# Performance work log

Hardware: AMD Instinct MI355X
Metric: run time of the kernel (lower is better)

Reference implementation:

```python
import jax, jax.numpy as jnp
from jax import lax
import numpy as np


def _lstm_scan(x, mask, w_ih, w_hh, b_ih, b_hh):
    # x: [S,B,E], mask: [S,B] bool. torch LSTM gate order: i,f,g,o.
    S, B, _ = x.shape
    H = w_hh.shape[1]
    def step(carry, inp):
        h, c = carry
        xt, mt = inp
        g = xt @ w_ih.T + h @ w_hh.T + b_ih + b_hh
        i, f, gg, o = jnp.split(g, 4, axis=-1)
        c_new = jax.nn.sigmoid(f) * c + jax.nn.sigmoid(i) * jnp.tanh(gg)
        h_new = jax.nn.sigmoid(o) * jnp.tanh(c_new)
        m = mt[:, None]
        return (jnp.where(m, h_new, h), jnp.where(m, c_new, c)), jnp.where(m, h_new, 0.0)
    init = (jnp.zeros((B, H), x.dtype), jnp.zeros((B, H), x.dtype))
    _, hs = lax.scan(step, init, (x, mask))
    return hs  # [S,B,H], zero at padded positions (matches pad_packed_sequence)


def _crf_nll(emissions, tags, mask, start, end, trans):
    # torchcrf CRF (batch_first) negative log-likelihood, reduction='sum'.
    em = jnp.transpose(emissions, (1, 0, 2))  # [S,B,T]
    tg = tags.T                                # [S,B]
    mk = mask.T                                # [S,B] bool
    B = em.shape[1]
    bidx = jnp.arange(B)
    # numerator: gold path score
    score0 = start[tg[0]] + em[0, bidx, tg[0]]
    def num_step(carry, inp):
        score, prev = carry
        e_t, t_t, m_t = inp
        s = score + (trans[prev, t_t] + e_t[bidx, t_t]) * m_t.astype(score.dtype)
        prev2 = jnp.where(m_t, t_t, prev)
        return (s, prev2), None
    (score, last), _ = lax.scan(num_step, (score0, tg[0]), (em[1:], tg[1:], mk[1:]))
    num = score + end[last]
    # denominator: forward algorithm (log partition)
    def den_step(alpha, inp):
        e_t, m_t = inp
        nxt = jax.nn.logsumexp(alpha[:, :, None] + trans[None] + e_t[:, None, :], axis=1)
        return jnp.where(m_t[:, None], nxt, alpha), None
    alpha, _ = lax.scan(den_step, start[None] + em[0], (em[1:], mk[1:]))
    den = jax.nn.logsumexp(alpha + end[None], axis=1)
    return jnp.sum(den - num)  # model returns -llh (sum over batch)


def setup_inputs() -> dict:
    key = jax.random.key(0)
    ks = jax.random.split(key, 20)
    B, S, V, E, H, T = 128, 512, 50000, 256, 512, 32
    sc = 0.05
    sents = jax.random.randint(ks[0], (B, S), 0, V)
    lengths = jax.random.randint(ks[1], (B,), 1, S + 1).at[0].set(S)
    tags = jax.random.randint(ks[2], (B, S), 0, T)
    mask = jnp.arange(S)[None, :] < lengths[:, None]
    return {
        "sents_tensor": sents,
        "lengths": lengths,
        "tags": tags,
        "mask": mask,
        "emb_table": jax.random.normal(ks[3], (V, E), jnp.float32) * sc,
        "w_ih_f": jax.random.normal(ks[4], (4 * H, E), jnp.float32) * sc,
        "w_hh_f": jax.random.normal(ks[5], (4 * H, H), jnp.float32) * sc,
        "b_ih_f": jax.random.normal(ks[6], (4 * H,), jnp.float32) * sc,
        "b_hh_f": jax.random.normal(ks[7], (4 * H,), jnp.float32) * sc,
        "w_ih_b": jax.random.normal(ks[8], (4 * H, E), jnp.float32) * sc,
        "w_hh_b": jax.random.normal(ks[9], (4 * H, H), jnp.float32) * sc,
        "b_ih_b": jax.random.normal(ks[10], (4 * H,), jnp.float32) * sc,
        "b_hh_b": jax.random.normal(ks[11], (4 * H,), jnp.float32) * sc,
        "lin_w": jax.random.normal(ks[12], (T, 2 * H), jnp.float32) * sc,
        "lin_b": jax.random.normal(ks[13], (T,), jnp.float32) * sc,
        "start_trans": jax.random.uniform(ks[14], (T,), jnp.float32, -0.1, 0.1),
        "end_trans": jax.random.uniform(ks[15], (T,), jnp.float32, -0.1, 0.1),
        "transitions": jax.random.uniform(ks[16], (T, T), jnp.float32, -0.1, 0.1),
    }


def reference(sents_tensor, lengths, tags, mask, emb_table,
              w_ih_f, w_hh_f, b_ih_f, b_hh_f,
              w_ih_b, w_hh_b, b_ih_b, b_hh_b,
              lin_w, lin_b, start_trans, end_trans, transitions):
    B, S = sents_tensor.shape
    emb = emb_table[sents_tensor]              # [B,S,E]
    xs = jnp.transpose(emb, (1, 0, 2))         # [S,B,E]
    mk = mask.T                                # [S,B]
    hs_f = _lstm_scan(xs, mk, w_ih_f, w_hh_f, b_ih_f, b_hh_f)
    # backward direction of packed BiLSTM: reverse each sequence within its length
    t = jnp.arange(S)[None, :]
    rev = jnp.where(t < lengths[:, None], lengths[:, None] - 1 - t, t)  # [B,S]
    x_rev = jnp.take_along_axis(emb, rev[:, :, None], axis=1)
    hs_b_rev = _lstm_scan(jnp.transpose(x_rev, (1, 0, 2)), mk, w_ih_b, w_hh_b, b_ih_b, b_hh_b)
    hs_b = jnp.take_along_axis(jnp.transpose(hs_b_rev, (1, 0, 2)), rev[:, :, None], axis=1)
    h = jnp.concatenate([jnp.transpose(hs_f, (1, 0, 2)), hs_b], axis=-1)  # [B,S,2H]
    # dropout in eval mode = identity
    logits = h @ lin_w.T + lin_b               # [B,S,T]
    return _crf_nll(logits, tags, mask, start_trans, end_trans, transitions)
```

## Files before the change

kernel.cpp:

```cpp
#include <hip/hip_runtime.h>
#include <hip/hip_bf16.h>
#include <cstdint>
#include <cstddef>

typedef __bf16 bf16;
typedef __bf16 bf16x8 __attribute__((ext_vector_type(8)));
typedef float f32x4 __attribute__((ext_vector_type(4)));

#define B_ 128
#define S_ 512
#define E_ 256
#define H_ 512

#define EMB_OFF   0UL
#define EMB_SZ    (128UL*512*256*2)
#define HSF_OFF   (EMB_OFF + EMB_SZ)
#define HS_SZ     (512UL*128*512*2)
#define HSB_OFF   (HSF_OFF + HS_SZ)
#define LOG_OFF   (HSB_OFF + HS_SZ)
#define LOG_SZ    (512UL*128*32*4)
#define HPING_OFF (LOG_OFF + LOG_SZ)
#define HPING_SZ  (16UL*2*16*512*2)
#define WLIN_OFF  (HPING_OFF + HPING_SZ)
#define WLIN_SZ   (32UL*1024*2)
#define BAR_OFF   ((WLIN_OFF + WLIN_SZ + 255UL) & ~255UL)
#define BAR_SZ    (16UL*16*32*4)

#define LD_AG(p)    __hip_atomic_load((p),  __ATOMIC_RELAXED, __HIP_MEMORY_SCOPE_AGENT)
#define ST_AG(p,v)  __hip_atomic_store((p), (v), __ATOMIC_RELAXED, __HIP_MEMORY_SCOPE_AGENT)

__device__ __forceinline__ float fsig(float x)  { return 1.0f / (1.0f + __expf(-x)); }
__device__ __forceinline__ float ftanhf(float x){ return 1.0f - 2.0f / (__expf(2.0f * x) + 1.0f); }

__global__ void embed_gather(const int* __restrict__ sents,
                             const float* __restrict__ table,
                             bf16* __restrict__ emb) {
    int t = threadIdx.x;
    int row = blockIdx.x * 8 + (t >> 5);
    int e0 = (t & 31) * 8;
    int idx = sents[row];
    const float4* src = (const float4*)(table + (size_t)idx * 256 + e0);
    float4 f0 = src[0], f1 = src[1];
    bf16x8 v;
    v[0]=(bf16)f0.x; v[1]=(bf16)f0.y; v[2]=(bf16)f0.z; v[3]=(bf16)f0.w;
    v[4]=(bf16)f1.x; v[5]=(bf16)f1.y; v[6]=(bf16)f1.z; v[7]=(bf16)f1.w;
    *(bf16x8*)(emb + (size_t)row * 256 + e0) = v;
}

__global__ void conv_linw(const float* __restrict__ w, bf16* __restrict__ o) {
    int i = blockIdx.x * 256 + threadIdx.x;
    o[i] = (bf16)w[i];
}

__global__ __launch_bounds__(256, 1) void lstm_persistent(
    const bf16* __restrict__ emb, bf16* __restrict__ hping,
    bf16* __restrict__ hs_f, bf16* __restrict__ hs_b,
    const float* __restrict__ w_ih_f, const float* __restrict__ w_hh_f,
    const float* __restrict__ b_ih_f, const float* __restrict__ b_hh_f,
    const float* __restrict__ w_ih_b, const float* __restrict__ w_hh_b,
    const float* __restrict__ b_ih_b, const float* __restrict__ b_hh_b,
    const int* __restrict__ lengths, int* __restrict__ bar)
{
    const int tid = threadIdx.x;
    const int l   = tid & 63;
    const int wv  = tid >> 6;
    const int bid = blockIdx.x;
    const int slot = bid >> 3;
    const int g  = (bid & 7) + ((slot >> 4) << 3);
    const int k  = slot & 15;
    const int d  = g >> 3;
    const int bg = g & 7;
    const int U0 = k * 32;

    const float* Wih = d ? w_ih_b : w_ih_f;
    const float* Whh = d ? w_hh_b : w_hh_f;
    const float* Bih = d ? b_ih_b : b_ih_f;
    const float* Bhh = d ? b_hh_b : b_hh_f;

    __shared__ uint4 smemA[1536];
    __shared__ float gatesS[16 * 132];
    __shared__ float c_sh[512];
    __shared__ float h_sh[512];
    __shared__ int   sh_tmax;

    bf16x8 wf[24][2];
    {
        const int lane15 = l & 15, q = l >> 4;
        #pragma unroll
        for (int kk = 0; kk < 24; ++kk) {
            #pragma unroll
            for (int T = 0; T < 2; ++T) {
                int c   = T * 16 + lane15;
                int row = (c >> 3) * 512 + U0 + 8 * wv + (c & 7);
                int k0  = kk * 32 + q * 8;
                const float* src = (k0 < 256) ? (Wih + (size_t)row * 256 + k0)
                                              : (Whh + (size_t)row * 512 + (k0 - 256));
                float4 f0 = *(const float4*)src;
                float4 f1 = *(const float4*)(src + 4);
                bf16x8 v;
                v[0]=(bf16)f0.x; v[1]=(bf16)f0.y; v[2]=(bf16)f0.z; v[3]=(bf16)f0.w;
                v[4]=(bf16)f1.x; v[5]=(bf16)f1.y; v[6]=(bf16)f1.z; v[7]=(bf16)f1.w;
                wf[kk][T] = v;
            }
        }
    }

    const int uu = tid & 31;
    const int ub = tid >> 5;
    float bI, bF, bG, bO;
    {
        int r0 = U0 + uu;
        bI = Bih[r0]        + Bhh[r0];
        bF = Bih[512 + r0]  + Bhh[512 + r0];
        bG = Bih[1024 + r0] + Bhh[1024 + r0];
        bO = Bih[1536 + r0] + Bhh[1536 + r0];
    }
    int lenU0 = lengths[bg * 16 + ub * 2];
    int lenU1 = lengths[bg * 16 + ub * 2 + 1];

    const int sr  = tid & 15;
    const int sc0 = tid >> 4;
    const int lenR = lengths[bg * 16 + sr];
    const bf16* embB = emb + ((size_t)(bg * 16 + sr)) * 512 * 256;

    for (int i = tid; i < 512; i += 256) { c_sh[i] = 0.0f; h_sh[i] = 0.0f; }
    bf16* hp = hping + (size_t)g * (2 * 16 * 512);
    {
        int r = tid >> 4, cc = tid & 15;
        unsigned int* p = (unsigned int*)(hp + r * 512 + U0 + cc * 2);
        ST_AG(p, 0u);
    }
    if (tid == 0) {
        int mx = 0;
        for (int b2 = 0; b2 < 16; ++b2) mx = max(mx, lengths[bg * 16 + b2]);
        sh_tmax = mx;
    }
    __builtin_amdgcn_s_waitcnt(0x0f70);
    __syncthreads();
    const int tmax = sh_tmax;

    int* slots  = bar + g * 16 * 32;
    int* myslot = slots + k * 32;
    int* pollp  = slots + (tid & 15) * 32;
    if (tid == 0) ST_AG(myslot, 1);

    const int sig = 4 * (l & 15) + (l >> 4);

    for (int t = 0; t < tmax; ++t) {
        bf16* hcur = hp + (t & 1) * (16 * 512);
        bf16* hnxt = hp + ((t + 1) & 1) * (16 * 512);

        int pos = (d == 0) ? t : ((t < lenR) ? (lenR - 1 - t) : t);
        const bf16* xsrc = embB + (size_t)pos * 256;
        #pragma unroll
        for (int i = 0; i < 2; ++i) {
            int c = sc0 + 16 * i;
            uint4 v = *(const uint4*)(xsrc + c * 8);
            smemA[((c >> 2) << 6) + 4 * sr + (c & 3)] = v;
        }

        if (tid < 16) {
            while (LD_AG(pollp) < t + 1) {}
        }
        __syncthreads();

        #pragma unroll
        for (int i = 2; i < 6; ++i) {
            int c = sc0 + 16 * i;
            unsigned int* src = (unsigned int*)(hcur + sr * 512 + (c - 32) * 8);
            uint4 v;
            v.x = LD_AG(src + 0);
            v.y = LD_AG(src + 1);
            v.z = LD_AG(src + 2);
            v.w = LD_AG(src + 3);
            smemA[((c >> 2) << 6) + 4 * sr + (c & 3)] = v;
        }
        __syncthreads();

        f32x4 acc0 = {0.f, 0.f, 0.f, 0.f}, acc1 = {0.f, 0.f, 0.f, 0.f};
        #pragma unroll
        for (int kk = 0; kk < 24; ++kk) {
            bf16x8 a = *(const bf16x8*)&smemA[(kk << 6) + sig];
            acc0 = __builtin_amdgcn_mfma_f32_16x16x32_bf16(a, wf[kk][0], acc0, 0, 0, 0);
            acc1 = __builtin_amdgcn_mfma_f32_16x16x32_bf16(a, wf[kk][1], acc1, 0, 0, 0);
        }
        {
            int c0l = l & 15;
            int colA = (wv << 5) + ((c0l & 7) << 2) + (c0l >> 3);
            int colB = colA + 2;
            int rbase = (l >> 4) * 4;
            #pragma unroll
            for (int reg = 0; reg < 4; ++reg) {
                gatesS[(rbase + reg) * 132 + colA] = acc0[reg];
                gatesS[(rbase + reg) * 132 + colB] = acc1[reg];
            }
        }
        __syncthreads();

        #pragma unroll
        for (int bi = 0; bi < 2; ++bi) {
            int b   = ub * 2 + bi;
            int len = bi ? lenU1 : lenU0;
            float4 gv = *(const float4*)&gatesS[b * 132 + ((uu >> 3) << 5) + ((uu & 7) << 2)];
            float iv = fsig(gv.x + bI);
            float fv = fsig(gv.y + bF);
            float gg = ftanhf(gv.z + bG);
            float ov = fsig(gv.w + bO);
            int si = b * 32 + uu;
            float co = c_sh[si], ho = h_sh[si];
            float cn = fv * co + iv * gg;
            float hn = ov * ftanhf(cn);
            bool m = (t < len);
            float cw = m ? cn : co;
            float hw = m ? hn : ho;
            c_sh[si] = cw; h_sh[si] = hw;
            bf16 hb = (bf16)hw;
            ST_AG((unsigned short*)(hnxt + b * 512 + U0 + uu),
                  __builtin_bit_cast(unsigned short, hb));
            if (d == 0) {
                hs_f[((size_t)t * 128 + bg * 16 + b) * 512 + U0 + uu] = hb;
            } else if (m) {
                hs_b[((size_t)(len - 1 - t) * 128 + bg * 16 + b) * 512 + U0 + uu] = hb;
            }
        }

        __builtin_amdgcn_s_waitcnt(0x0f70);
        __syncthreads();
        if (tid == 0) ST_AG(myslot, t + 2);
    }
}

__global__ __launch_bounds__(256) void logits_kernel(
    const bf16* __restrict__ hs_f, const bf16* __restrict__ hs_b,
    const bf16* __restrict__ wlin, const float* __restrict__ lin_b,
    float* __restrict__ logits)
{
    const int tid = threadIdx.x;
    const int l = tid & 63, wv = tid >> 6;
    const int m = l & 15, q = l >> 4;
    const size_t R0 = (size_t)blockIdx.x * 64 + wv * 16;
    const size_t rowA = (R0 + m) * 512;
    f32x4 acc0 = {0.f,0.f,0.f,0.f}, acc1 = {0.f,0.f,0.f,0.f};
    #pragma unroll
    for (int kk = 0; kk < 32; ++kk) {
        int k0 = kk * 32 + q * 8;
        const bf16* asrc = (k0 < 512) ? (hs_f + rowA + k0) : (hs_b + rowA + (k0 - 512));
        bf16x8 a  = *(const bf16x8*)asrc;
        bf16x8 b0 = *(const bf16x8*)(wlin + (size_t)m * 1024 + k0);
        bf16x8 b1 = *(const bf16x8*)(wlin + (size_t)(16 + m) * 1024 + k0);
        acc0 = __builtin_amdgcn_mfma_f32_16x16x32_bf16(a, b0, acc0, 0, 0, 0);
        acc1 = __builtin_amdgcn_mfma_f32_16x16x32_bf16(a, b1, acc1, 0, 0, 0);
    }
    float lb0 = lin_b[m], lb1 = lin_b[16 + m];
    #pragma unroll
    for (int reg = 0; reg < 4; ++reg) {
        size_t row = R0 + q * 4 + reg;
        logits[row * 32 + m]      = acc0[reg] + lb0;
        logits[row * 32 + 16 + m] = acc1[reg] + lb1;
    }
}

__global__ void crf_kernel(const float* __restrict__ logits,
                           const int* __restrict__ tags, const int* __restrict__ lengths,
                           const float* __restrict__ startt, const float* __restrict__ endt,
                           const float* __restrict__ trans, float* __restrict__ out)
{
    const int b = blockIdx.x;
    const int l = threadIdx.x;
    const int j = l & 31, hh = l >> 5;
    const int len = lengths[b];
    const int* tg = tags + b * 512;

    float s = 0.0f;
    for (int t = 1 + l; t < len; t += 64) {
        int pt = tg[t - 1], ct = tg[t];
        s += trans[pt * 32 + ct] + logits[((size_t)t * 128 + b) * 32 + ct];
    }
    #pragma unroll
    for (int off = 32; off > 0; off >>= 1) s += __shfl_xor(s, off, 64);
    float num = s + startt[tg[0]] + logits[(size_t)b * 32 + tg[0]];

    float Tc[16];
    #pragma unroll
    for (int ii = 0; ii < 16; ++ii) Tc[ii] = trans[(hh * 16 + ii) * 32 + j];
    float alpha = startt[j] + logits[(size_t)b * 32 + j];
    for (int t = 1; t < len; ++t) {
        float e = logits[((size_t)t * 128 + b) * 32 + j];
        float v[16];
        #pragma unroll
        for (int ii = 0; ii < 16; ++ii) v[ii] = __shfl(alpha, hh * 16 + ii, 64) + Tc[ii];
        float mx = v[0];
        #pragma unroll
        for (int ii = 1; ii < 16; ++ii) mx = fmaxf(mx, v[ii]);
        mx = fmaxf(mx, __shfl_xor(mx, 32, 64));
        float sm = 0.0f;
        #pragma unroll
        for (int ii = 0; ii < 16; ++ii) sm += __expf(v[ii] - mx);
        sm += __shfl_xor(sm, 32, 64);
        alpha = e + mx + __logf(sm);
    }
    float fvv = alpha + endt[j];
    float mx = fvv;
    #pragma unroll
    for (int off = 16; off > 0; off >>= 1) mx = fmaxf(mx, __shfl_xor(mx, off, 64));
    float sm = __expf(fvv - mx);
    #pragma unroll
    for (int off = 16; off > 0; off >>= 1) sm += __shfl_xor(sm, off, 64);
    float den = mx + __logf(sm);
    if (l == 0) atomicAdd(out, den - num);
}

extern "C" void kernel_launch(void* const* d_in, const int* in_sizes, int n_in,
                              void* d_out, int out_size, void* d_ws, size_t ws_size,
                              hipStream_t stream) {
    const int*   sents   = (const int*)d_in[0];
    const int*   lengths = (const int*)d_in[1];
    const int*   tags    = (const int*)d_in[2];
    const float* table   = (const float*)d_in[4];
    const float* w_ih_f  = (const float*)d_in[5];
    const float* w_hh_f  = (const float*)d_in[6];
    const float* b_ih_f  = (const float*)d_in[7];
    const float* b_hh_f  = (const float*)d_in[8];
    const float* w_ih_b  = (const float*)d_in[9];
    const float* w_hh_b  = (const float*)d_in[10];
    const float* b_ih_b  = (const float*)d_in[11];
    const float* b_hh_b  = (const float*)d_in[12];
    const float* lin_w   = (const float*)d_in[13];
    const float* lin_b   = (const float*)d_in[14];
    const float* startt  = (const float*)d_in[15];
    const float* endt    = (const float*)d_in[16];
    const float* trans   = (const float*)d_in[17];

    char* wsb = (char*)d_ws;
    bf16*  emb    = (bf16*)(wsb + EMB_OFF);
    bf16*  hs_f   = (bf16*)(wsb + HSF_OFF);
    bf16*  hs_b   = (bf16*)(wsb + HSB_OFF);
    float* logits = (float*)(wsb + LOG_OFF);
    bf16*  hping  = (bf16*)(wsb + HPING_OFF);
    bf16*  wlin   = (bf16*)(wsb + WLIN_OFF);
    int*   bar    = (int*)(wsb + BAR_OFF);

    hipMemsetAsync(d_out, 0, sizeof(float), stream);
    hipMemsetAsync(bar, 0, BAR_SZ, stream);

    embed_gather<<<8192, 256, 0, stream>>>(sents, table, emb);
    conv_linw<<<128, 256, 0, stream>>>(lin_w, wlin);

    void* args[] = { &emb, &hping, &hs_f, &hs_b,
                     &w_ih_f, &w_hh_f, &b_ih_f, &b_hh_f,
                     &w_ih_b, &w_hh_b, &b_ih_b, &b_hh_b,
                     &lengths, &bar };
    hipError_t e = hipLaunchCooperativeKernel((const void*)lstm_persistent,
                                              dim3(256), dim3(256), args, 0, stream);
    if (e != hipSuccess) {
        lstm_persistent<<<256, 256, 0, stream>>>(emb, hping, hs_f, hs_b,
            w_ih_f, w_hh_f, b_ih_f, b_hh_f, w_ih_b, w_hh_b, b_ih_b, b_hh_b,
            lengths, bar);
    }

    logits_kernel<<<1024, 256, 0, stream>>>(hs_f, hs_b, wlin, lin_b, logits);
    crf_kernel<<<128, 64, 0, stream>>>(logits, tags, lengths, startt, endt, trans,
                                       (float*)d_out);
}
```

Baseline: 2.823 ms.

## Replace flag barrier with step-tagged hidden-state words in persistent LSTM

Each hidden-state element is now stored as a 32-bit word whose upper 16 bits hold the timestep tag and lower 16 bits hold the bf16 value. Consumers spin on the data itself until every word carries the expected tag. This removes the per-step slot-counter barrier, the extra waitcnt/syncthreads and the flag write. Separately, the CRF forward loop now prefetches the next emission value. The cost is doubled traffic for the h exchange and wider polling loads. Words left in the workspace from a previous run could carry stale tags that happen to match, since the buffer is no longer zeroed.

New measurement: 4.922 ms. 74.3% more time.

```diff
diff --git a/kernel.cpp b/kernel.cpp
--- a/kernel.cpp
+++ b/kernel.cpp
@@ -19,12 +19,10 @@
 #define HSB_OFF   (HSF_OFF + HS_SZ)
 #define LOG_OFF   (HSB_OFF + HS_SZ)
 #define LOG_SZ    (512UL*128*32*4)
-#define HPING_OFF (LOG_OFF + LOG_SZ)
-#define HPING_SZ  (16UL*2*16*512*2)
-#define WLIN_OFF  (HPING_OFF + HPING_SZ)
+#define TAG_OFF   (LOG_OFF + LOG_SZ)
+#define TAG_SZ    (16UL*2*16*512*4)
+#define WLIN_OFF  (TAG_OFF + TAG_SZ)
 #define WLIN_SZ   (32UL*1024*2)
-#define BAR_OFF   ((WLIN_OFF + WLIN_SZ + 255UL) & ~255UL)
-#define BAR_SZ    (16UL*16*32*4)
 
 #define LD_AG(p)    __hip_atomic_load((p),  __ATOMIC_RELAXED, __HIP_MEMORY_SCOPE_AGENT)
 #define ST_AG(p,v)  __hip_atomic_store((p), (v), __ATOMIC_RELAXED, __HIP_MEMORY_SCOPE_AGENT)
@@ -53,13 +51,13 @@
 }
 
 __global__ __launch_bounds__(256, 1) void lstm_persistent(
-    const bf16* __restrict__ emb, bf16* __restrict__ hping,
+    const bf16* __restrict__ emb, unsigned* __restrict__ tagged,
     bf16* __restrict__ hs_f, bf16* __restrict__ hs_b,
     const float* __restrict__ w_ih_f, const float* __restrict__ w_hh_f,
     const float* __restrict__ b_ih_f, const float* __restrict__ b_hh_f,
     const float* __restrict__ w_ih_b, const float* __restrict__ w_hh_b,
     const float* __restrict__ b_ih_b, const float* __restrict__ b_hh_b,
-    const int* __restrict__ lengths, int* __restrict__ bar)
+    const int* __restrict__ lengths)
 {
     const int tid = threadIdx.x;
     const int l   = tid & 63;
@@ -117,63 +115,63 @@
     }
     int lenU0 = lengths[bg * 16 + ub * 2];
     int lenU1 = lengths[bg * 16 + ub * 2 + 1];
+    unsigned* tagBase = tagged + (size_t)g * 16384;
+    unsigned* tagW0 = tagBase + (ub * 2) * 512 + U0 + uu;
+    unsigned* tagW1 = tagBase + (ub * 2 + 1) * 512 + U0 + uu;
 
     const int sr  = tid & 15;
-    const int sc0 = tid >> 4;
+    const int sc0v = tid >> 4;
     const int lenR = lengths[bg * 16 + sr];
     const bf16* embB = emb + ((size_t)(bg * 16 + sr)) * 512 * 256;
+    const unsigned* tgpBase = tagBase + sr * 512 + sc0v * 32;
 
     for (int i = tid; i < 512; i += 256) { c_sh[i] = 0.0f; h_sh[i] = 0.0f; }
-    bf16* hp = hping + (size_t)g * (2 * 16 * 512);
-    {
-        int r = tid >> 4, cc = tid & 15;
-        unsigned int* p = (unsigned int*)(hp + r * 512 + U0 + cc * 2);
-        ST_AG(p, 0u);
-    }
     if (tid == 0) {
         int mx = 0;
         for (int b2 = 0; b2 < 16; ++b2) mx = max(mx, lengths[bg * 16 + b2]);
         sh_tmax = mx;
     }
-    __builtin_amdgcn_s_waitcnt(0x0f70);
     __syncthreads();
     const int tmax = sh_tmax;
 
-    int* slots  = bar + g * 16 * 32;
-    int* myslot = slots + k * 32;
-    int* pollp  = slots + (tid & 15) * 32;
-    if (tid == 0) ST_AG(myslot, 1);
-
     const int sig = 4 * (l & 15) + (l >> 4);
 
     for (int t = 0; t < tmax; ++t) {
-        bf16* hcur = hp + (t & 1) * (16 * 512);
-        bf16* hnxt = hp + ((t + 1) & 1) * (16 * 512);
-
         int pos = (d == 0) ? t : ((t < lenR) ? (lenR - 1 - t) : t);
         const bf16* xsrc = embB + (size_t)pos * 256;
         #pragma unroll
         for (int i = 0; i < 2; ++i) {
-            int c = sc0 + 16 * i;
+            int c = sc0v + 16 * i;
             uint4 v = *(const uint4*)(xsrc + c * 8);
             smemA[((c >> 2) << 6) + 4 * sr + (c & 3)] = v;
         }
 
-        if (tid < 16) {
-            while (LD_AG(pollp) < t + 1) {}
-        }
-        __syncthreads();
-
-        #pragma unroll
-        for (int i = 2; i < 6; ++i) {
-            int c = sc0 + 16 * i;
-            unsigned int* src = (unsigned int*)(hcur + sr * 512 + (c - 32) * 8);
-            uint4 v;
-            v.x = LD_AG(src + 0);
-            v.y = LD_AG(src + 1);
-            v.z = LD_AG(src + 2);
-            v.w = LD_AG(src + 3);
-            smemA[((c >> 2) << 6) + 4 * sr + (c & 3)] = v;
+        if (t == 0) {
+            uint4 z = {0u, 0u, 0u, 0u};
+            #pragma unroll
+            for (int i = 0; i < 4; ++i)
+                smemA[((8 + sc0v) << 6) + 4 * sr + i] = z;
+        } else {
+            const unsigned need = (unsigned)t << 16;
+            const unsigned* tgp = tgpBase + (t & 1) * 8192;
+            unsigned w[32];
+            for (;;) {
+                #pragma unroll
+                for (int j = 0; j < 32; ++j) w[j] = LD_AG(tgp + j);
+                bool ok = true;
+                #pragma unroll
+                for (int j = 0; j < 32; ++j) ok &= ((w[j] & 0xffff0000u) == need);
+                if (ok) break;
+            }
+            #pragma unroll
+            for (int i = 0; i < 4; ++i) {
+                uint4 q;
+                q.x = (w[8*i+0] & 0xffffu) | (w[8*i+1] << 16);
+                q.y = (w[8*i+2] & 0xffffu) | (w[8*i+3] << 16);
+                q.z = (w[8*i+4] & 0xffffu) | (w[8*i+5] << 16);
+                q.w = (w[8*i+6] & 0xffffu) | (w[8*i+7] << 16);
+                smemA[((8 + sc0v) << 6) + 4 * sr + i] = q;
+            }
         }
         __syncthreads();
 
@@ -197,6 +195,8 @@
         }
         __syncthreads();
 
+        const unsigned ntag = (unsigned)(t + 1) << 16;
+        const int npar = ((t + 1) & 1) * 8192;
         #pragma unroll
         for (int bi = 0; bi < 2; ++bi) {
             int b   = ub * 2 + bi;
@@ -215,18 +215,14 @@
             float hw = m ? hn : ho;
             c_sh[si] = cw; h_sh[si] = hw;
             bf16 hb = (bf16)hw;
-            ST_AG((unsigned short*)(hnxt + b * 512 + U0 + uu),
-                  __builtin_bit_cast(unsigned short, hb));
+            unsigned hbits = (unsigned)__builtin_bit_cast(unsigned short, hb);
+            ST_AG((bi ? tagW1 : tagW0) + npar, ntag | hbits);
             if (d == 0) {
                 hs_f[((size_t)t * 128 + bg * 16 + b) * 512 + U0 + uu] = hb;
             } else if (m) {
                 hs_b[((size_t)(len - 1 - t) * 128 + bg * 16 + b) * 512 + U0 + uu] = hb;
             }
         }
-
-        __builtin_amdgcn_s_waitcnt(0x0f70);
-        __syncthreads();
-        if (tid == 0) ST_AG(myslot, t + 2);
     }
 }
 
@@ -284,8 +280,10 @@
     #pragma unroll
     for (int ii = 0; ii < 16; ++ii) Tc[ii] = trans[(hh * 16 + ii) * 32 + j];
     float alpha = startt[j] + logits[(size_t)b * 32 + j];
+    float e_next = (len > 1) ? logits[((size_t)1 * 128 + b) * 32 + j] : 0.0f;
     for (int t = 1; t < len; ++t) {
-        float e = logits[((size_t)t * 128 + b) * 32 + j];
+        float e = e_next;
+        if (t + 1 < len) e_next = logits[((size_t)(t + 1) * 128 + b) * 32 + j];
         float v[16];
         #pragma unroll
         for (int ii = 0; ii < 16; ++ii) v[ii] = __shfl(alpha, hh * 16 + ii, 64) + Tc[ii];
@@ -332,30 +330,28 @@
     const float* trans   = (const float*)d_in[17];
 
     char* wsb = (char*)d_ws;
-    bf16*  emb    = (bf16*)(wsb + EMB_OFF);
-    bf16*  hs_f   = (bf16*)(wsb + HSF_OFF);
-    bf16*  hs_b   = (bf16*)(wsb + HSB_OFF);
-    float* logits = (float*)(wsb + LOG_OFF);
-    bf16*  hping  = (bf16*)(wsb + HPING_OFF);
-    bf16*  wlin   = (bf16*)(wsb + WLIN_OFF);
-    int*   bar    = (int*)(wsb + BAR_OFF);
+    bf16*     emb    = (bf16*)(wsb + EMB_OFF);
+    bf16*     hs_f   = (bf16*)(wsb + HSF_OFF);
+    bf16*     hs_b   = (bf16*)(wsb + HSB_OFF);
+    float*    logits = (float*)(wsb + LOG_OFF);
+    unsigned* tagged = (unsigned*)(wsb + TAG_OFF);
+    bf16*     wlin   = (bf16*)(wsb + WLIN_OFF);
 
     hipMemsetAsync(d_out, 0, sizeof(float), stream);
-    hipMemsetAsync(bar, 0, BAR_SZ, stream);
 
     embed_gather<<<8192, 256, 0, stream>>>(sents, table, emb);
     conv_linw<<<128, 256, 0, stream>>>(lin_w, wlin);
 
-    void* args[] = { &emb, &hping, &hs_f, &hs_b,
+    void* args[] = { &emb, &tagged, &hs_f, &hs_b,
                      &w_ih_f, &w_hh_f, &b_ih_f, &b_hh_f,
                      &w_ih_b, &w_hh_b, &b_ih_b, &b_hh_b,
-                     &lengths, &bar };
+                     &lengths };
     hipError_t e = hipLaunchCooperativeKernel((const void*)lstm_persistent,
                                               dim3(256), dim3(256), args, 0, stream);
     if (e != hipSuccess) {
-        lstm_persistent<<<256, 256, 0, stream>>>(emb, hping, hs_f, hs_b,
+        lstm_persistent<<<256, 256, 0, stream>>>(emb, tagged, hs_f, hs_b,
             w_ih_f, w_hh_f, b_ih_f, b_hh_f, w_ih_b, w_hh_b, b_ih_b, b_hh_b,
-            lengths, bar);
+            lengths);
     }
 
     logits_kernel<<<1024, 256, 0, stream>>>(hs_f, hs_b, wlin, lin_b, logits);
```
